# Kernel optimization log

Hardware: AMD Instinct MI355X
Metric: run time of the kernel (lower is better)

## Reference

```python
import jax, jax.numpy as jnp
import numpy as np

SEQ_LEN = 512
NUM_FEATURES = 16
BATCH = 8
D_MODEL = 512
TOP_K = 5
MAX_P = 512  # largest patch size == seq_len
LAMBD = 0.01


def get_patch_sizes(seq_len):
    # torch: 1/rfftfreq(L)[1:], floor, unique (desc), [::-1] -> ascending unique periods
    freqs = np.fft.rfftfreq(seq_len)[1:]
    periods = np.floor(1.0 / freqs).astype(np.int64)
    return [int(p) for p in np.unique(periods)]


def _sinusoid(n, d):
    pos = np.arange(n, dtype=np.float64)[:, None]
    i = np.arange(d, dtype=np.float64)[None, :]
    angle = pos / np.power(10000.0, (2.0 * np.floor(i / 2.0)) / d)
    return np.where((np.arange(d)[None, :] % 2) == 0, np.sin(angle), np.cos(angle))


def pos_emb_2d(d_model, C, N):
    # 2D sinusoidal positional embedding over (feature idx, patch idx):
    # first half of d_model encodes the feature dim, second half the patch position.
    half = d_model // 2
    pe_feat = _sinusoid(C, half)              # [C, half]
    pe_pos = _sinusoid(N, d_model - half)     # [N, d_model-half]
    pe = np.concatenate([
        np.broadcast_to(pe_feat[:, None, :], (C, N, half)),
        np.broadcast_to(pe_pos[None, :, :], (C, N, d_model - half)),
    ], axis=-1)
    return jnp.asarray(pe, dtype=jnp.float32)  # [C, N, d_model]


def softshrink(x, lambd=LAMBD):
    return jnp.where(x > lambd, x - lambd, jnp.where(x < -lambd, x + lambd, jnp.zeros_like(x)))


def _forward(x, w_start, b_start, w1, b1, w2, b2, w_gate, Wv):
    B, L, C = x.shape
    patch_sizes = get_patch_sizes(L)
    # ---- AFNO1D gating (eval mode: clean logits, no noise) ----
    xs = (x @ w_start)[..., 0] + b_start[0]           # start_fc -> [B, L]
    xf = jnp.fft.rfft(xs, norm='ortho')[:, 1:]        # drop DC -> [B, F], F = L//2
    xr, xi = jnp.real(xf), jnp.imag(xf)
    o1r = jax.nn.relu(xr @ w1[0] - xi @ w1[1] + b1[0])
    o1i = jax.nn.relu(xi @ w1[0] + xr @ w1[1] + b1[1])
    o2r = softshrink(o1r @ w2[0] - o1i @ w2[1] + b2[0])
    o2i = softshrink(o1i @ w2[0] + o1r @ w2[1] + b2[1])
    amp = jnp.sqrt(o2r * o2r + o2i * o2i + 1e-12)     # |complex|, eps for grad safety at 0
    logits = amp @ w_gate                             # [B, E]
    top_w, top_i = jax.lax.top_k(logits, TOP_K)
    top_w = jax.nn.softmax(top_w, axis=-1)
    gates = jnp.zeros_like(logits).at[jnp.arange(B)[:, None], top_i].set(top_w)
    # ---- per-patch-size embedding (dense dispatch: unrouted rows zeroed) ----
    xt = jnp.swapaxes(x, 1, 2)                        # [B, C, L]
    outs = []
    for i, p in enumerate(patch_sizes):               # static loop over 43 experts
        n = -(-L // p)                                # ceil(L / p)
        xp = jnp.pad(xt, ((0, 0), (0, 0), (0, n * p - L)), mode='edge')  # ReplicationPad1d
        patches = xp.reshape(B, C, n, p)              # unfold(-1, p, p)
        emb = jnp.einsum('bcnp,pd->bcnd', patches, Wv[i, :p, :])
        emb = emb + pos_emb_2d(D_MODEL, C, n)[None]
        mask = (gates[:, i] > 0).astype(emb.dtype)
        outs.append(emb * mask[:, None, None, None])
    emb_all = jnp.concatenate(outs, axis=2)           # [B, C, total_patches, d_model]
    return emb_all, gates


def setup_inputs():
    key = jax.random.key(0)
    ks = jax.random.split(key, 8)
    L, C, D = SEQ_LEN, NUM_FEATURES, D_MODEL
    F = L // 2
    E = len(get_patch_sizes(L))
    scale = 1.0 / D
    x = jax.random.normal(ks[0], (BATCH, L, C), jnp.float32)
    w_start = jax.random.normal(ks[1], (C, 1), jnp.float32) / float(np.sqrt(C))
    b_start = jnp.zeros((1,), jnp.float32)
    w1 = scale * jax.random.normal(ks[2], (2, F, 4 * F), jnp.float32)
    b1 = scale * jax.random.normal(ks[3], (2, 4 * F), jnp.float32)
    w2 = scale * jax.random.normal(ks[4], (2, 4 * F, F), jnp.float32)
    b2 = scale * jax.random.normal(ks[5], (2, F), jnp.float32)
    w_gate = 0.01 * jax.random.normal(ks[6], (F, E), jnp.float32)  # randn (not zeros) for nontrivial routing
    Wv = jax.random.normal(ks[7], (E, MAX_P, D), jnp.float32) / float(np.sqrt(MAX_P))  # padded per-expert Linear(p, d_model) weights; expert i uses Wv[i, :p_i]
    return {"x": x, "w_start": w_start, "b_start": b_start, "w1": w1, "b1": b1,
            "w2": w2, "b2": b2, "w_gate": w_gate, "Wv": Wv}


def reference(x, w_start, b_start, w1, b1, w2, b2, w_gate, Wv):
    return _forward(x, w_start, b_start, w1, b1, w2, b2, w_gate, Wv)
```

## Files before the change

kernel.cpp:

```cpp
#include <hip/hip_runtime.h>
#include <math.h>


typedef float v4f __attribute__((ext_vector_type(4)));

constexpr int NEXP = 43;
constexpr int NTOT = 1657;
constexpr long long GATES_OFF = 108593152LL;

constexpr int WS_XR  = 0;
constexpr int WS_XI  = 2048;
constexpr int WS_O1R = 4096;
constexpr int WS_O1I = 12288;
constexpr int WS_P2  = 20480;
constexpr int WS_PEF = 53248;
constexpr int WS_PEP = 57344;

struct Tables { int P[NEXP], N[NEXP], G0[NEXP], ne; };

constexpr Tables make_tables() {
  Tables t{};
  int ne = 0;
  for (int p = 2; p <= 512; ++p) {
    int k = 512 / p;
    if (k >= 1 && 512 / k == p) t.P[ne++] = p;
  }
  t.ne = ne;
  int g = 0;
  for (int i = 0; i < ne; ++i) {
    int p = t.P[i], n = (512 + p - 1) / p;
    t.N[i] = n; t.G0[i] = g; g += n;
  }
  return t;
}
constexpr Tables HTBL = make_tables();
static_assert(HTBL.ne == 43, "expert count");
static_assert(HTBL.G0[42] + HTBL.N[42] == NTOT, "total patches");

constexpr int CHUNK_P = 64;
constexpr int count_chunks() {
  int c = 0;
  for (int i = 0; i < HTBL.ne; ++i) c += (HTBL.N[i] + CHUNK_P - 1) / CHUNK_P;
  return c;
}
constexpr int NCHUNK = count_chunks();
static_assert(NCHUNK == 52, "chunk count");

struct Chunks { int v[NCHUNK]; };
constexpr Chunks make_chunks() {
  Chunks c{}; int idx = 0;
  for (int i = 0; i < HTBL.ne; ++i) {
    int n = HTBL.N[i];
    for (int m0 = 0; m0 < n; m0 += CHUNK_P) {
      int mc = (n - m0 < CHUNK_P) ? (n - m0) : CHUNK_P;
      c.v[idx++] = i | (m0 << 6) | (mc << 15);
    }
  }
  return c;
}
__constant__ Tables TBLC = make_tables();
__constant__ Chunks CHKC = make_chunks();

__global__ void k_pre(const float* __restrict__ x, const float* __restrict__ w_start,
                      const float* __restrict__ b_start, float* __restrict__ ws) {
  if (blockIdx.x < 8) {
    __shared__ float xs[512];
    int b = blockIdx.x, t = threadIdx.x;
    float w[16];
#pragma unroll
    for (int c = 0; c < 16; ++c) w[c] = w_start[c];
    float bs = b_start[0];
    for (int l = t; l < 512; l += 256) {
      const float* xp = x + ((size_t)b * 512 + l) * 16;
      float s = bs;
#pragma unroll
      for (int c = 0; c < 16; ++c) s = fmaf(xp[c], w[c], s);
      xs[l] = s;
    }
    __syncthreads();
    int k = t + 1;
    float ar = 0.f, ai = 0.f;
    int ph = 0;
    for (int l = 0; l < 512; ++l) {
      float a = (float)ph * (1.0f / 256.0f);
      float v = xs[l];
      ar = fmaf(v,  cospif(a), ar);
      ai = fmaf(-v, sinpif(a), ai);
      ph = (ph + k) & 511;
    }
    const float sc = 0.044194173824159216f;
    ws[WS_XR + b * 256 + t] = ar * sc;
    ws[WS_XI + b * 256 + t] = ai * sc;
  } else {
    int idx = (blockIdx.x - 8) * 256 + threadIdx.x;
    const float K = 0.03597789207803197f;
    if (idx < 4096) {
      int c = idx >> 8, d = idx & 255;
      float ang = (float)c * expf(-(float)(d & ~1) * K);
      ws[WS_PEF + idx] = (d & 1) ? cosf(ang) : sinf(ang);
    } else {
      int r = idx - 4096, mm = r >> 8, j = r & 255;
      float ang = (float)mm * expf(-(float)(j & ~1) * K);
      ws[WS_PEP + r] = (j & 1) ? cosf(ang) : sinf(ang);
    }
  }
}

__global__ void k_fc1(const float* __restrict__ w1, const float* __restrict__ b1,
                      float* __restrict__ ws) {
  __shared__ float xr[256], xi[256];
  int b = blockIdx.x >> 2, jg = blockIdx.x & 3, t = threadIdx.x;
  xr[t] = ws[WS_XR + b * 256 + t];
  xi[t] = ws[WS_XI + b * 256 + t];
  __syncthreads();
  int j = jg * 256 + t;
  float s_ra = 0.f, s_rb = 0.f, s_ia = 0.f, s_ib = 0.f;
  for (int k = 0; k < 256; ++k) {
    float a  = w1[k * 1024 + j];
    float bb = w1[262144 + k * 1024 + j];
    float r = xr[k], im = xi[k];
    s_ra = fmaf(r, a, s_ra);  s_ib = fmaf(im, bb, s_ib);
    s_ia = fmaf(im, a, s_ia); s_rb = fmaf(r, bb, s_rb);
  }
  ws[WS_O1R + b * 1024 + j] = fmaxf(s_ra - s_ib + b1[j], 0.f);
  ws[WS_O1I + b * 1024 + j] = fmaxf(s_ia + s_rb + b1[1024 + j], 0.f);
}

__global__ void k_fc2a(const float* __restrict__ w2, float* __restrict__ ws) {
  __shared__ float lr[256], li[256];
  int b = blockIdx.x >> 2, kc = blockIdx.x & 3, t = threadIdx.x;
  lr[t] = ws[WS_O1R + b * 1024 + kc * 256 + t];
  li[t] = ws[WS_O1I + b * 1024 + kc * 256 + t];
  __syncthreads();
  float s_rr = 0.f, s_ri = 0.f, s_ir = 0.f, s_ii = 0.f;
  int kb = kc * 256;
  for (int k = 0; k < 256; ++k) {
    float a  = w2[(kb + k) * 256 + t];
    float bb = w2[262144 + (kb + k) * 256 + t];
    float r = lr[k], im = li[k];
    s_rr = fmaf(r, a, s_rr);  s_ii = fmaf(im, bb, s_ii);
    s_ir = fmaf(im, a, s_ir); s_ri = fmaf(r, bb, s_ri);
  }
  float* P = ws + WS_P2 + (size_t)(b * 4 + kc) * 1024 + t;
  P[0] = s_rr; P[256] = s_ii; P[512] = s_ir; P[768] = s_ri;
}

__device__ __forceinline__ float softshrink(float v) {
  const float l = 0.01f;
  return v > l ? v - l : (v < -l ? v + l : 0.f);
}

__global__ void k_fc2b(const float* __restrict__ b2, const float* __restrict__ w_gate,
                       float* __restrict__ ws, float* __restrict__ out) {
  __shared__ float amp[256], lg[64];
  int b = blockIdx.x, t = threadIdx.x;
  float s_rr = 0.f, s_ii = 0.f, s_ir = 0.f, s_ri = 0.f;
  for (int kc = 0; kc < 4; ++kc) {
    const float* P = ws + WS_P2 + (size_t)(b * 4 + kc) * 1024 + t;
    s_rr += P[0]; s_ii += P[256]; s_ir += P[512]; s_ri += P[768];
  }
  float o2r = softshrink(s_rr - s_ii + b2[t]);
  float o2i = softshrink(s_ir + s_ri + b2[256 + t]);
  amp[t] = sqrtf(o2r * o2r + o2i * o2i + 1e-12f);
  __syncthreads();
  if (t < NEXP) {
    float s = 0.f;
    for (int k = 0; k < 256; ++k) s = fmaf(amp[k], w_gate[k * NEXP + t], s);
    lg[t] = s;
  }
  __syncthreads();
  if (t == 0) {
    float v[NEXP];
    for (int e = 0; e < NEXP; ++e) v[e] = lg[e];
    float vals[5]; int idx[5];
    for (int r = 0; r < 5; ++r) {
      float best = -INFINITY; int bi = 0;
      for (int e = 0; e < NEXP; ++e)
        if (v[e] > best) { best = v[e]; bi = e; }
      vals[r] = best; idx[r] = bi; v[bi] = -INFINITY;
    }
    float den = 0.f, wv[5];
    for (int r = 0; r < 5; ++r) { wv[r] = expf(vals[r] - vals[0]); den += wv[r]; }
    float g[NEXP];
    for (int e = 0; e < NEXP; ++e) g[e] = 0.f;
    for (int r = 0; r < 5; ++r) g[idx[r]] = wv[r] / den;
    for (int e = 0; e < NEXP; ++e) out[GATES_OFF + (size_t)b * NEXP + e] = g[e];
  }
}

__device__ __forceinline__ v4f fma4(float xv, v4f w, v4f a) {
  a.x = fmaf(xv, w.x, a.x);
  a.y = fmaf(xv, w.y, a.y);
  a.z = fmaf(xv, w.z, a.z);
  a.w = fmaf(xv, w.w, a.w);
  return a;
}

__global__ __launch_bounds__(256)
void k_main(const float* __restrict__ x, const float* __restrict__ Wv,
            const float* __restrict__ ws, float* __restrict__ out) {
  int desc = CHKC.v[blockIdx.x];
  int i = desc & 63, m0 = (desc >> 6) & 511, mc = desc >> 15;
  int bc = blockIdx.y, b = bc >> 4, c = bc & 15;
  int t = threadIdx.x;

  float gate = out[GATES_OFF + (size_t)b * NEXP + i];
  int g0 = TBLC.G0[i] + m0;
  size_t base = ((size_t)bc * NTOT + g0) * 512;

  if (gate <= 0.f) {
    v4f z = {0.f, 0.f, 0.f, 0.f};
    v4f* o = (v4f*)(out + base);
    int nv = mc * 128;
    for (int v = t; v < nv; v += 256)
      __builtin_nontemporal_store(z, o + v);
    return;
  }

  int p = TBLC.P[i];
  __shared__ float xl[512];
  for (int l = t; l < 512; l += 256)
    xl[l] = x[((size_t)b * 512 + l) * 16 + c];
  __syncthreads();

  int dg = t & 127, d0 = dg * 4, ps = t >> 7;
  const float* wp = Wv + (size_t)i * 262144 + d0;
  bool lo = (d0 < 256);
  v4f pef = {0.f, 0.f, 0.f, 0.f};
  if (lo) pef = *(const v4f*)(ws + WS_PEF + c * 256 + d0);

  for (int mm = ps; mm < mc; mm += 2) {
    int m = m0 + mm;
    int lb = m * p;
    v4f a0 = {0.f,0.f,0.f,0.f}, a1 = {0.f,0.f,0.f,0.f};
    v4f a2 = {0.f,0.f,0.f,0.f}, a3 = {0.f,0.f,0.f,0.f};
    int q = 0;
    for (; q + 4 <= p; q += 4) {
      int l0 = lb + q,     l1 = lb + q + 1, l2 = lb + q + 2, l3 = lb + q + 3;
      l0 = l0 > 511 ? 511 : l0;  l1 = l1 > 511 ? 511 : l1;
      l2 = l2 > 511 ? 511 : l2;  l3 = l3 > 511 ? 511 : l3;
      const float* wq = wp + (size_t)q * 512;
      v4f w0 = *(const v4f*)(wq);
      v4f w1v = *(const v4f*)(wq + 512);
      v4f w2v = *(const v4f*)(wq + 1024);
      v4f w3v = *(const v4f*)(wq + 1536);
      a0 = fma4(xl[l0], w0,  a0);
      a1 = fma4(xl[l1], w1v, a1);
      a2 = fma4(xl[l2], w2v, a2);
      a3 = fma4(xl[l3], w3v, a3);
    }
    for (; q < p; ++q) {
      int l = lb + q; l = l > 511 ? 511 : l;
      a0 = fma4(xl[l], *(const v4f*)(wp + (size_t)q * 512), a0);
    }
    v4f acc = (a0 + a1) + (a2 + a3);
    v4f pe = lo ? pef : *(const v4f*)(ws + WS_PEP + m * 256 + (d0 - 256));
    v4f r = acc + pe;
    __builtin_nontemporal_store(r, (v4f*)(out + base + (size_t)mm * 512 + d0));
  }
}

extern "C" void kernel_launch(void* const* d_in, const int* in_sizes, int n_in,
                              void* d_out, int out_size, void* d_ws, size_t ws_size,
                              hipStream_t stream) {
  const float* x       = (const float*)d_in[0];
  const float* w_start = (const float*)d_in[1];
  const float* b_start = (const float*)d_in[2];
  const float* w1      = (const float*)d_in[3];
  const float* b1      = (const float*)d_in[4];
  const float* w2      = (const float*)d_in[5];
  const float* b2      = (const float*)d_in[6];
  const float* w_gate  = (const float*)d_in[7];
  const float* Wv      = (const float*)d_in[8];
  float* out = (float*)d_out;
  float* ws  = (float*)d_ws;

  k_pre  <<<280, 256, 0, stream>>>(x, w_start, b_start, ws);
  k_fc1  <<<32,  256, 0, stream>>>(w1, b1, ws);
  k_fc2a <<<32,  256, 0, stream>>>(w2, ws);
  k_fc2b <<<8,   256, 0, stream>>>(b2, w_gate, ws, out);
  k_main <<<dim3(NCHUNK, 128), 256, 0, stream>>>(x, Wv, ws, out);
}
```

Before: 592.2 us.

## Fuse gating pipeline into one kernel with atomic last-block reduction

The four small gating kernels (start_fc+DFT, fc1, fc2 partial, fc2 reduce + top-k) become one 32-block kernel. Each block recomputes the per-batch DFT and uses a shared twiddle table instead of per-iteration cospif/sinpif. The last block per batch, chosen by an atomic counter, does the reduction and routing. Positional embeddings are now computed inline in k_main with sinf/cosf instead of loaded from a precomputed workspace, which removes launches but adds transcendental work per output vector.

```diff
diff --git a/kernel.cpp b/kernel.cpp
--- a/kernel.cpp
+++ b/kernel.cpp
@@ -8,13 +8,8 @@
 constexpr int NTOT = 1657;
 constexpr long long GATES_OFF = 108593152LL;
 
-constexpr int WS_XR  = 0;
-constexpr int WS_XI  = 2048;
-constexpr int WS_O1R = 4096;
-constexpr int WS_O1I = 12288;
 constexpr int WS_P2  = 20480;
-constexpr int WS_PEF = 53248;
-constexpr int WS_PEP = 57344;
+constexpr int WS_CNT = 53248;
 
 struct Tables { int P[NEXP], N[NEXP], G0[NEXP], ne; };
 
@@ -61,11 +56,31 @@
 __constant__ Tables TBLC = make_tables();
 __constant__ Chunks CHKC = make_chunks();
 
-__global__ void k_pre(const float* __restrict__ x, const float* __restrict__ w_start,
-                      const float* __restrict__ b_start, float* __restrict__ ws) {
-  if (blockIdx.x < 8) {
-    __shared__ float xs[512];
-    int b = blockIdx.x, t = threadIdx.x;
+__global__ void k_init(float* __restrict__ ws) {
+  if (threadIdx.x < 8) ((unsigned*)(ws + WS_CNT))[threadIdx.x] = 0u;
+}
+
+__device__ __forceinline__ float softshrink(float v) {
+  const float l = 0.01f;
+  return v > l ? v - l : (v < -l ? v + l : 0.f);
+}
+
+__global__ __launch_bounds__(256)
+void k_fused(const float* __restrict__ x, const float* __restrict__ w_start,
+             const float* __restrict__ b_start, const float* __restrict__ w1,
+             const float* __restrict__ b1, const float* __restrict__ w2,
+             const float* __restrict__ b2, const float* __restrict__ w_gate,
+             float* __restrict__ ws, float* __restrict__ out) {
+  __shared__ float xs[512];
+  __shared__ float2 tw[512];
+  __shared__ float xr[256], xi[256];
+  __shared__ float lr[256], li[256];
+  __shared__ float amp[256], lg[64];
+  __shared__ int lastflag;
+
+  int bx = blockIdx.x, b = bx >> 2, g = bx & 3, t = threadIdx.x;
+
+  {
     float w[16];
 #pragma unroll
     for (int c = 0; c < 16; ++c) w[c] = w_start[c];
@@ -76,92 +91,77 @@
 #pragma unroll
       for (int c = 0; c < 16; ++c) s = fmaf(xp[c], w[c], s);
       xs[l] = s;
-    }
-    __syncthreads();
+      float a = (float)l * (1.0f / 256.0f);
+      tw[l] = make_float2(cospif(a), sinpif(a));
+    }
+  }
+  __syncthreads();
+
+  {
     int k = t + 1;
     float ar = 0.f, ai = 0.f;
     int ph = 0;
     for (int l = 0; l < 512; ++l) {
-      float a = (float)ph * (1.0f / 256.0f);
       float v = xs[l];
-      ar = fmaf(v,  cospif(a), ar);
-      ai = fmaf(-v, sinpif(a), ai);
+      float2 wv = tw[ph];
+      ar = fmaf(v,  wv.x, ar);
+      ai = fmaf(-v, wv.y, ai);
       ph = (ph + k) & 511;
     }
     const float sc = 0.044194173824159216f;
-    ws[WS_XR + b * 256 + t] = ar * sc;
-    ws[WS_XI + b * 256 + t] = ai * sc;
-  } else {
-    int idx = (blockIdx.x - 8) * 256 + threadIdx.x;
-    const float K = 0.03597789207803197f;
-    if (idx < 4096) {
-      int c = idx >> 8, d = idx & 255;
-      float ang = (float)c * expf(-(float)(d & ~1) * K);
-      ws[WS_PEF + idx] = (d & 1) ? cosf(ang) : sinf(ang);
-    } else {
-      int r = idx - 4096, mm = r >> 8, j = r & 255;
-      float ang = (float)mm * expf(-(float)(j & ~1) * K);
-      ws[WS_PEP + r] = (j & 1) ? cosf(ang) : sinf(ang);
-    }
-  }
-}
-
-__global__ void k_fc1(const float* __restrict__ w1, const float* __restrict__ b1,
-                      float* __restrict__ ws) {
-  __shared__ float xr[256], xi[256];
-  int b = blockIdx.x >> 2, jg = blockIdx.x & 3, t = threadIdx.x;
-  xr[t] = ws[WS_XR + b * 256 + t];
-  xi[t] = ws[WS_XI + b * 256 + t];
-  __syncthreads();
-  int j = jg * 256 + t;
-  float s_ra = 0.f, s_rb = 0.f, s_ia = 0.f, s_ib = 0.f;
-  for (int k = 0; k < 256; ++k) {
-    float a  = w1[k * 1024 + j];
-    float bb = w1[262144 + k * 1024 + j];
-    float r = xr[k], im = xi[k];
-    s_ra = fmaf(r, a, s_ra);  s_ib = fmaf(im, bb, s_ib);
-    s_ia = fmaf(im, a, s_ia); s_rb = fmaf(r, bb, s_rb);
-  }
-  ws[WS_O1R + b * 1024 + j] = fmaxf(s_ra - s_ib + b1[j], 0.f);
-  ws[WS_O1I + b * 1024 + j] = fmaxf(s_ia + s_rb + b1[1024 + j], 0.f);
-}
-
-__global__ void k_fc2a(const float* __restrict__ w2, float* __restrict__ ws) {
-  __shared__ float lr[256], li[256];
-  int b = blockIdx.x >> 2, kc = blockIdx.x & 3, t = threadIdx.x;
-  lr[t] = ws[WS_O1R + b * 1024 + kc * 256 + t];
-  li[t] = ws[WS_O1I + b * 1024 + kc * 256 + t];
-  __syncthreads();
-  float s_rr = 0.f, s_ri = 0.f, s_ir = 0.f, s_ii = 0.f;
-  int kb = kc * 256;
-  for (int k = 0; k < 256; ++k) {
-    float a  = w2[(kb + k) * 256 + t];
-    float bb = w2[262144 + (kb + k) * 256 + t];
-    float r = lr[k], im = li[k];
-    s_rr = fmaf(r, a, s_rr);  s_ii = fmaf(im, bb, s_ii);
-    s_ir = fmaf(im, a, s_ir); s_ri = fmaf(r, bb, s_ri);
-  }
-  float* P = ws + WS_P2 + (size_t)(b * 4 + kc) * 1024 + t;
-  P[0] = s_rr; P[256] = s_ii; P[512] = s_ir; P[768] = s_ri;
-}
-
-__device__ __forceinline__ float softshrink(float v) {
-  const float l = 0.01f;
-  return v > l ? v - l : (v < -l ? v + l : 0.f);
-}
-
-__global__ void k_fc2b(const float* __restrict__ b2, const float* __restrict__ w_gate,
-                       float* __restrict__ ws, float* __restrict__ out) {
-  __shared__ float amp[256], lg[64];
-  int b = blockIdx.x, t = threadIdx.x;
-  float s_rr = 0.f, s_ii = 0.f, s_ir = 0.f, s_ri = 0.f;
-  for (int kc = 0; kc < 4; ++kc) {
-    const float* P = ws + WS_P2 + (size_t)(b * 4 + kc) * 1024 + t;
-    s_rr += P[0]; s_ii += P[256]; s_ir += P[512]; s_ri += P[768];
-  }
-  float o2r = softshrink(s_rr - s_ii + b2[t]);
-  float o2i = softshrink(s_ir + s_ri + b2[256 + t]);
-  amp[t] = sqrtf(o2r * o2r + o2i * o2i + 1e-12f);
+    xr[t] = ar * sc;
+    xi[t] = ai * sc;
+  }
+  __syncthreads();
+
+  int j = g * 256 + t;
+  {
+    float s_ra = 0.f, s_rb = 0.f, s_ia = 0.f, s_ib = 0.f;
+    for (int k = 0; k < 256; ++k) {
+      float a  = w1[k * 1024 + j];
+      float bb = w1[262144 + k * 1024 + j];
+      float r = xr[k], im = xi[k];
+      s_ra = fmaf(r, a, s_ra);  s_ib = fmaf(im, bb, s_ib);
+      s_ia = fmaf(im, a, s_ia); s_rb = fmaf(r, bb, s_rb);
+    }
+    lr[t] = fmaxf(s_ra - s_ib + b1[j], 0.f);
+    li[t] = fmaxf(s_ia + s_rb + b1[1024 + j], 0.f);
+  }
+  __syncthreads();
+
+  {
+    float s_rr = 0.f, s_ri = 0.f, s_ir = 0.f, s_ii = 0.f;
+    int kb = g * 256;
+    for (int k = 0; k < 256; ++k) {
+      float a  = w2[(kb + k) * 256 + t];
+      float bb = w2[262144 + (kb + k) * 256 + t];
+      float r = lr[k], im = li[k];
+      s_rr = fmaf(r, a, s_rr);  s_ii = fmaf(im, bb, s_ii);
+      s_ir = fmaf(im, a, s_ir); s_ri = fmaf(r, bb, s_ri);
+    }
+    float* P = ws + WS_P2 + (size_t)(b * 4 + g) * 1024 + t;
+    P[0] = s_rr; P[256] = s_ii; P[512] = s_ir; P[768] = s_ri;
+  }
+  __threadfence();
+  __syncthreads();
+  if (t == 0) {
+    unsigned old = atomicAdd((unsigned*)(ws + WS_CNT) + b, 1u);
+    lastflag = (old == 3u);
+  }
+  __syncthreads();
+  if (!lastflag) return;
+  __threadfence();
+
+  {
+    float rr = 0.f, ii = 0.f, ir = 0.f, ri = 0.f;
+    for (int kc = 0; kc < 4; ++kc) {
+      const float* Q = ws + WS_P2 + (size_t)(b * 4 + kc) * 1024 + t;
+      rr += Q[0]; ii += Q[256]; ir += Q[512]; ri += Q[768];
+    }
+    float o2r = softshrink(rr - ii + b2[t]);
+    float o2i = softshrink(ir + ri + b2[256 + t]);
+    amp[t] = sqrtf(o2r * o2r + o2i * o2i + 1e-12f);
+  }
   __syncthreads();
   if (t < NEXP) {
     float s = 0.f;
@@ -181,10 +181,10 @@
     }
     float den = 0.f, wv[5];
     for (int r = 0; r < 5; ++r) { wv[r] = expf(vals[r] - vals[0]); den += wv[r]; }
-    float g[NEXP];
-    for (int e = 0; e < NEXP; ++e) g[e] = 0.f;
-    for (int r = 0; r < 5; ++r) g[idx[r]] = wv[r] / den;
-    for (int e = 0; e < NEXP; ++e) out[GATES_OFF + (size_t)b * NEXP + e] = g[e];
+    float gt[NEXP];
+    for (int e = 0; e < NEXP; ++e) gt[e] = 0.f;
+    for (int r = 0; r < 5; ++r) gt[idx[r]] = wv[r] / den;
+    for (int e = 0; e < NEXP; ++e) out[GATES_OFF + (size_t)b * NEXP + e] = gt[e];
   }
 }
 
@@ -198,7 +198,7 @@
 
 __global__ __launch_bounds__(256)
 void k_main(const float* __restrict__ x, const float* __restrict__ Wv,
-            const float* __restrict__ ws, float* __restrict__ out) {
+            float* __restrict__ out) {
   int desc = CHKC.v[blockIdx.x];
   int i = desc & 63, m0 = (desc >> 6) & 511, mc = desc >> 15;
   int bc = blockIdx.y, b = bc >> 4, c = bc & 15;
@@ -226,8 +226,21 @@
   int dg = t & 127, d0 = dg * 4, ps = t >> 7;
   const float* wp = Wv + (size_t)i * 262144 + d0;
   bool lo = (d0 < 256);
+
+  const float K = 0.03597789207803197f;
   v4f pef = {0.f, 0.f, 0.f, 0.f};
-  if (lo) pef = *(const v4f*)(ws + WS_PEF + c * 256 + d0);
+  float e0 = 0.f, e1 = 0.f;
+  if (lo) {
+    float f0 = expf(-(float)d0 * K);
+    float f1 = expf(-(float)(d0 + 2) * K);
+    float a0 = (float)c * f0, a1 = (float)c * f1;
+    pef.x = sinf(a0); pef.y = cosf(a0);
+    pef.z = sinf(a1); pef.w = cosf(a1);
+  } else {
+    int j0 = d0 - 256;
+    e0 = expf(-(float)j0 * K);
+    e1 = expf(-(float)(j0 + 2) * K);
+  }
 
   for (int mm = ps; mm < mc; mm += 2) {
     int m = m0 + mm;
@@ -254,7 +267,14 @@
       a0 = fma4(xl[l], *(const v4f*)(wp + (size_t)q * 512), a0);
     }
     v4f acc = (a0 + a1) + (a2 + a3);
-    v4f pe = lo ? pef : *(const v4f*)(ws + WS_PEP + m * 256 + (d0 - 256));
+    v4f pe;
+    if (lo) {
+      pe = pef;
+    } else {
+      float b0 = (float)m * e0, b1v = (float)m * e1;
+      pe.x = sinf(b0);  pe.y = cosf(b0);
+      pe.z = sinf(b1v); pe.w = cosf(b1v);
+    }
     v4f r = acc + pe;
     __builtin_nontemporal_store(r, (v4f*)(out + base + (size_t)mm * 512 + d0));
   }
@@ -275,9 +295,7 @@
   float* out = (float*)d_out;
   float* ws  = (float*)d_ws;
 
-  k_pre  <<<280, 256, 0, stream>>>(x, w_start, b_start, ws);
-  k_fc1  <<<32,  256, 0, stream>>>(w1, b1, ws);
-  k_fc2a <<<32,  256, 0, stream>>>(w2, ws);
-  k_fc2b <<<8,   256, 0, stream>>>(b2, w_gate, ws, out);
-  k_main <<<dim3(NCHUNK, 128), 256, 0, stream>>>(x, Wv, ws, out);
-}
+  k_init  <<<1, 64, 0, stream>>>(ws);
+  k_fused <<<32, 256, 0, stream>>>(x, w_start, b_start, w1, b1, w2, b2, w_gate, ws, out);
+  k_main  <<<dim3(NCHUNK, 128), 256, 0, stream>>>(x, Wv, out);
+}
```

Result: faster. 566.8 us (-4.3%).
